# Performance work log

Hardware: AMD Instinct MI355X
Metric: run time of the kernel (lower is better)

## Reference

```python
import jax, jax.numpy as jnp
import numpy as np

L, C = 32768, 512
EPS = 1e-5

def _layernorm(x, w, b):
    mu = jnp.mean(x, axis=-1, keepdims=True)
    var = jnp.mean(jnp.square(x - mu), axis=-1, keepdims=True)
    return (x - mu) * jax.lax.rsqrt(var + EPS) * w + b

def _scan(u, decay):
    # inclusive first-order linear scan: b_t = decay * b_{t-1} + u_t
    a = jnp.broadcast_to(decay, u.shape)
    def combine(l, r):
        return (l[0] * r[0], r[1] + r[0] * l[1])
    _, b = jax.lax.associative_scan(combine, (a, u), axis=0)
    return b

def setup_inputs() -> dict:
    key = jax.random.key(0)
    ks = jax.random.split(key, 8)
    s = 0.02
    return {
        "x": jax.random.normal(ks[0], (L, C), dtype=jnp.float32),
        "ln1_w": jnp.ones((C,), jnp.float32),
        "ln1_b": jnp.zeros((C,), jnp.float32),
        "W_in": jax.random.normal(ks[1], (C, C), jnp.float32) * s,
        "b_in": jnp.zeros((C,), jnp.float32),
        "W_gate": jax.random.normal(ks[2], (C, C), jnp.float32) * s,
        "b_gate": jnp.zeros((C,), jnp.float32),
        "W_out": jax.random.normal(ks[3], (C, C), jnp.float32) * s,
        "b_out": jnp.zeros((C,), jnp.float32),
        "decay_logit": jnp.zeros((C,), jnp.float32),  # torch init: zeros -> sigmoid = 0.5
        "ln2_w": jnp.ones((C,), jnp.float32),
        "ln2_b": jnp.zeros((C,), jnp.float32),
        "W_ff1": jax.random.normal(ks[4], (C, 2 * C), jnp.float32) * s,
        "b_ff1": jnp.zeros((2 * C,), jnp.float32),
        "W_ff2": jax.random.normal(ks[5], (2 * C, C), jnp.float32) * s,
        "b_ff2": jnp.zeros((C,), jnp.float32),
    }

def reference(x, ln1_w, ln1_b, W_in, b_in, W_gate, b_gate, W_out, b_out,
              decay_logit, ln2_w, ln2_b, W_ff1, b_ff1, W_ff2, b_ff2):
    hidden = _layernorm(x, ln1_w, ln1_b)
    u = hidden @ W_in + b_in
    gate = jax.nn.sigmoid(hidden @ W_gate + b_gate)
    decay = jax.nn.sigmoid(decay_logit)
    fwd = _scan(u, decay) * gate
    bwd = jnp.flip(_scan(jnp.flip(u, axis=0), decay), axis=0) * gate
    state_out = 0.5 * (fwd + bwd)
    x = x + state_out @ W_out + b_out
    h = _layernorm(x, ln2_w, ln2_b)
    x = x + jax.nn.silu(h @ W_ff1 + b_ff1) @ W_ff2 + b_ff2
    return x
```

## Files before the change

kernel.cpp:

```cpp
#include <hip/hip_runtime.h>
#include <stdint.h>


#define L_SEQ 32768
#define CDIM 512
#define LN_EPS 1e-5f
#define CHUNK 64
#define NCHUNK (L_SEQ / CHUNK)
#define NGRP 16
#define GCHUNK (NCHUNK / NGRP)

typedef __attribute__((ext_vector_type(8))) short short8;
typedef __attribute__((ext_vector_type(4))) float floatx4;

__device__ inline unsigned short f2bf(float f) {
  union { float f; unsigned int u; } v; v.f = f;
  unsigned int r = v.u + 0x7fffu + ((v.u >> 16) & 1u);
  return (unsigned short)(r >> 16);
}
__device__ inline float bf2f(unsigned short h) {
  union { float f; unsigned int u; } v; v.u = ((unsigned int)h) << 16;
  return v.f;
}
__device__ inline float sigmoidf_(float x) { return 1.0f / (1.0f + __expf(-x)); }

__device__ inline float powi5(float s, int e) {
  float p = 1.f;
#pragma unroll
  for (int b = 0; b < 5; b++) { if (e & (1 << b)) p *= s; s *= s; }
  return p;
}

__device__ __forceinline__ void gll16(const void* g, void* l) {
  __builtin_amdgcn_global_load_lds(
      (__attribute__((address_space(1))) void*)g,
      (__attribute__((address_space(3))) void*)l, 16, 0, 0);
}

__global__ __launch_bounds__(256) void ln_kernel(const float* __restrict__ x,
    const float* __restrict__ w, const float* __restrict__ b,
    unsigned short* __restrict__ out) {
  int row = blockIdx.x * 4 + (threadIdx.x >> 6);
  int lane = threadIdx.x & 63;
  const float4* xr = (const float4*)(x + (size_t)row * CDIM);
  float4 v0 = xr[lane * 2];
  float4 v1 = xr[lane * 2 + 1];
  float s = v0.x + v0.y + v0.z + v0.w + v1.x + v1.y + v1.z + v1.w;
  float s2 = v0.x * v0.x + v0.y * v0.y + v0.z * v0.z + v0.w * v0.w +
             v1.x * v1.x + v1.y * v1.y + v1.z * v1.z + v1.w * v1.w;
  for (int m = 32; m > 0; m >>= 1) {
    s += __shfl_xor(s, m, 64);
    s2 += __shfl_xor(s2, m, 64);
  }
  float mean = s * (1.0f / CDIM);
  float var = s2 * (1.0f / CDIM) - mean * mean;
  float rs = rsqrtf(var + LN_EPS);
  const float4* wr = (const float4*)w;
  const float4* br = (const float4*)b;
  float4 w0 = wr[lane * 2], w1 = wr[lane * 2 + 1];
  float4 b0 = br[lane * 2], b1 = br[lane * 2 + 1];
  unsigned int p0 = (unsigned int)f2bf((v0.x - mean) * rs * w0.x + b0.x) |
                    ((unsigned int)f2bf((v0.y - mean) * rs * w0.y + b0.y) << 16);
  unsigned int p1 = (unsigned int)f2bf((v0.z - mean) * rs * w0.z + b0.z) |
                    ((unsigned int)f2bf((v0.w - mean) * rs * w0.w + b0.w) << 16);
  unsigned int p2 = (unsigned int)f2bf((v1.x - mean) * rs * w1.x + b1.x) |
                    ((unsigned int)f2bf((v1.y - mean) * rs * w1.y + b1.y) << 16);
  unsigned int p3 = (unsigned int)f2bf((v1.z - mean) * rs * w1.z + b1.z) |
                    ((unsigned int)f2bf((v1.w - mean) * rs * w1.w + b1.w) << 16);
  uint4 pk; pk.x = p0; pk.y = p1; pk.z = p2; pk.w = p3;
  *((uint4*)(out + (size_t)row * CDIM + lane * 8)) = pk;
}

__global__ __launch_bounds__(256) void prep_all(
    const float* __restrict__ W_in, const float* __restrict__ W_gate,
    const float* __restrict__ W_out, const float* __restrict__ W_ff1,
    const float* __restrict__ W_ff2, const float* __restrict__ logit,
    unsigned short* __restrict__ Wt_ig, unsigned short* __restrict__ Wt_out,
    unsigned short* __restrict__ Wt_ff1, unsigned short* __restrict__ Wt_ff2,
    float* __restrict__ decay, float* __restrict__ decayT) {
  int b = blockIdx.x;
  if (b >= 1792) {
    for (int c = threadIdx.x; c < CDIM; c += 256) {
      float d = sigmoidf_(logit[c]);
      decay[c] = d;
      float p = d;
      for (int i = 0; i < 6; i++) p *= p;
      decayT[c] = p;
    }
    return;
  }
  const float* W; unsigned short* Wt; int Kd, Nd, t;
  if (b < 256)       { W = W_in;   Wt = Wt_ig;             Kd = 512;  Nd = 512;  t = b; }
  else if (b < 512)  { W = W_gate; Wt = Wt_ig + 512 * 512; Kd = 512;  Nd = 512;  t = b - 256; }
  else if (b < 768)  { W = W_out;  Wt = Wt_out;            Kd = 512;  Nd = 512;  t = b - 512; }
  else if (b < 1280) { W = W_ff1;  Wt = Wt_ff1;            Kd = 512;  Nd = 1024; t = b - 768; }
  else               { W = W_ff2;  Wt = Wt_ff2;            Kd = 1024; Nd = 512;  t = b - 1280; }
  int ntx = Nd >> 5;
  int n0 = (t % ntx) * 32, k0 = (t / ntx) * 32;
  __shared__ float tile[32][33];
  int tx = threadIdx.x & 31, ty = threadIdx.x >> 5;
  for (int r = 0; r < 32; r += 8)
    tile[ty + r][tx] = W[(size_t)(k0 + ty + r) * Nd + n0 + tx];
  __syncthreads();
  for (int r = 0; r < 32; r += 8)
    Wt[(size_t)(n0 + ty + r) * Kd + k0 + tx] = f2bf(tile[tx][ty + r]);
}

template <int EPI>
__global__ __launch_bounds__(256, 4) void gemm_bt(
    const unsigned short* __restrict__ A, const unsigned short* __restrict__ Bt,
    const float* __restrict__ biasA, const float* __restrict__ biasB,
    const float* __restrict__ res, float* __restrict__ outF,
    unsigned short* __restrict__ outU, unsigned short* __restrict__ outG,
    const float* __restrict__ decayP, float* __restrict__ faP,
    float* __restrict__ baP, int M, int N, int K) {
  __shared__ char smemRaw[34048];
  unsigned short* As = (unsigned short*)smemRaw;
  unsigned short* Bs = (unsigned short*)(smemRaw + 16384);

  int nbx = gridDim.x, nby = gridDim.y;
  int bid = blockIdx.x + blockIdx.y * nbx;
  int per = (nbx * nby) >> 3;
  int w = (bid & 7) * per + (bid >> 3);
  int ni = w % nby;
  int mi = w / nby;
  int bm = mi << 7, bn = ni << 7;

  int tid = threadIdx.x, wave = tid >> 6, lane = tid & 63;
  int wm = (wave >> 1) * 64, wn = (wave & 1) * 64;

  int srow = wave * 16 + (lane >> 2);
  int chunkSel = (lane & 3) ^ ((lane >> 3) & 3);
  int scol = chunkSel * 8;
  const unsigned short* aP0 = A + (size_t)(bm + srow) * K + scol;
  const unsigned short* aP1 = A + (size_t)(bm + 64 + srow) * K + scol;
  const unsigned short* bP0 = Bt + (size_t)(bn + srow) * K + scol;
  const unsigned short* bP1 = Bt + (size_t)(bn + 64 + srow) * K + scol;
  int wbase = wave * 512;

#define STAGE(bufOff, ktile) do {                                 \
    int _o = (ktile) * 32;                                        \
    gll16(aP0 + _o, As + (bufOff) + wbase);                       \
    gll16(aP1 + _o, As + (bufOff) + 2048 + wbase);                \
    gll16(bP0 + _o, Bs + (bufOff) + wbase);                       \
    gll16(bP1 + _o, Bs + (bufOff) + 2048 + wbase);                \
  } while (0)

  floatx4 acc[4][4];
#pragma unroll
  for (int i = 0; i < 4; i++)
#pragma unroll
    for (int j = 0; j < 4; j++) acc[i][j] = (floatx4){0.f, 0.f, 0.f, 0.f};

  int quad = lane >> 4, r16 = lane & 15;
  int cSwz = ((quad ^ (r16 >> 1)) & 3) * 8;

  int NK = K >> 5;

  STAGE(0, 0);
  asm volatile("s_waitcnt vmcnt(0)" ::: "memory");
  __syncthreads();

  for (int k = 0; k < NK; ++k) {
    int cur = (k & 1) * 4096, nxt = cur ^ 4096;
    if (k + 1 < NK) STAGE(nxt, k + 1);
    short8 af[4], bfm[4];
#pragma unroll
    for (int i = 0; i < 4; i++)
      af[i] = *(const short8*)(&As[cur + (wm + i * 16 + r16) * 32 + cSwz]);
#pragma unroll
    for (int j = 0; j < 4; j++)
      bfm[j] = *(const short8*)(&Bs[cur + (wn + j * 16 + r16) * 32 + cSwz]);
#pragma unroll
    for (int i = 0; i < 4; i++)
#pragma unroll
      for (int j = 0; j < 4; j++)
        acc[i][j] = __builtin_amdgcn_mfma_f32_16x16x32_bf16(af[i], bfm[j], acc[i][j], 0, 0, 0);
    asm volatile("s_waitcnt vmcnt(0)" ::: "memory");
    __syncthreads();
  }
#undef STAGE

  if (EPI == 1) {
#pragma unroll
    for (int j = 0; j < 4; j++) {
      int n = bn + wn + j * 16 + r16;
#pragma unroll
      for (int i = 0; i < 4; i++) {
        int mb = bm + wm + i * 16 + quad * 4;
#pragma unroll
        for (int r = 0; r < 4; r++) {
          size_t idx = (size_t)(mb + r) * N + n;
          outF[idx] = res[idx] + acc[i][j][r] + biasA[n];
        }
      }
    }
  } else {
    unsigned short* sm = (unsigned short*)smemRaw;
#pragma unroll
    for (int j = 0; j < 4; j++) {
      int n = bn + wn + j * 16 + r16;
      int ln = wn + j * 16 + r16;
#pragma unroll
      for (int i = 0; i < 4; i++) {
        int lmb = wm + i * 16 + quad * 4;
#pragma unroll
        for (int r = 0; r < 4; r++) {
          float v = acc[i][j][r];
          float t;
          if (EPI == 0) {
            t = (n < 512) ? (v + biasA[n]) : sigmoidf_(v + biasB[n - 512]);
          } else {
            float z = v + biasA[n];
            t = z * sigmoidf_(z);
          }
          sm[(lmb + r) * 132 + ln] = f2bf(t);
        }
      }
    }
    __syncthreads();
    int row = tid >> 1, half = tid & 1;
    const unsigned short* src = sm + row * 132 + half * 64;
    unsigned short* gptr;
    if (EPI == 0) {
      gptr = ((bn < 512) ? outU : (outG - 512)) + (size_t)(bm + row) * 512 + bn + half * 64;
    } else {
      gptr = outG + (size_t)(bm + row) * N + bn + half * 64;
    }
#pragma unroll
    for (int s = 0; s < 8; s++)
      *(short8*)(gptr + s * 8) = *(const short8*)(src + s * 8);

    if (EPI == 0 && bn < 512 && faP != nullptr) {
      int cl = tid & 127;
      int ch = tid >> 7;
      int cg = bn + cl;
      float d = decayP[cg];
      const unsigned short* col = sm + (ch * 64) * 132 + cl;
      float f = 0.f, bs = 0.f, p = 1.f;
#pragma unroll 8
      for (int t = 0; t < CHUNK; t++) {
        float v = bf2f(col[t * 132]);
        f = d * f + v;
        bs += p * v;
        p *= d;
      }
      size_t kidx = (size_t)((bm >> 6) + ch) * CDIM + cg;
      faP[kidx] = f;
      baP[kidx] = bs;
    }
  }
}

__global__ __launch_bounds__(512) void scan_p2a(const float* __restrict__ fa,
    const float* __restrict__ ba, const float* __restrict__ decayT,
    float* __restrict__ fc, float* __restrict__ bc,
    float* __restrict__ gaF, float* __restrict__ gaB) {
  int c = threadIdx.x, g = blockIdx.x;
  float dT = decayT[c];
  int k0 = g * GCHUNK;
  float runf = 0.f;
#pragma unroll 4
  for (int j = 0; j < GCHUNK; j++) {
    size_t idx = (size_t)(k0 + j) * CDIM + c;
    fc[idx] = runf;
    runf = dT * runf + fa[idx];
  }
  gaF[(size_t)g * CDIM + c] = runf;
  float runb = 0.f;
#pragma unroll 4
  for (int j = GCHUNK - 1; j >= 0; j--) {
    size_t idx = (size_t)(k0 + j) * CDIM + c;
    bc[idx] = runb;
    runb = dT * runb + ba[idx];
  }
  gaB[(size_t)g * CDIM + c] = runb;
}

__global__ __launch_bounds__(512) void scan_p2b(const float* __restrict__ gaF,
    const float* __restrict__ gaB, const float* __restrict__ decayT,
    float* __restrict__ GF, float* __restrict__ GB) {
  int c = threadIdx.x;
  float dT = decayT[c];
  float d32 = dT;
#pragma unroll
  for (int i = 0; i < 5; i++) d32 *= d32;
  float gf = 0.f;
#pragma unroll
  for (int g = 0; g < NGRP; g++) {
    GF[(size_t)g * CDIM + c] = gf;
    gf = d32 * gf + gaF[(size_t)g * CDIM + c];
  }
  float gb = 0.f;
#pragma unroll
  for (int g = NGRP - 1; g >= 0; g--) {
    GB[(size_t)g * CDIM + c] = gb;
    gb = d32 * gb + gaB[(size_t)g * CDIM + c];
  }
}

__global__ __launch_bounds__(512) void scan_phase3(const unsigned short* __restrict__ u,
    const unsigned short* __restrict__ gate, const float* __restrict__ decay,
    const float* __restrict__ decayT, const float* __restrict__ fc,
    const float* __restrict__ bc, const float* __restrict__ GF,
    const float* __restrict__ GB, unsigned short* __restrict__ state) {
  int c = threadIdx.x, k = blockIdx.x;
  int g = k >> 5, j = k & 31;
  float d = decay[c];
  float dT = decayT[c];
  size_t base = (size_t)k * CHUNK * CDIM + c;
  size_t kc = (size_t)k * CDIM + c;
  size_t gc = (size_t)g * CDIM + c;
  float run  = fc[kc] + powi5(dT, j) * GF[gc];
  float runb0 = bc[kc] + powi5(dT, 31 - j) * GB[gc];
  float fwd[CHUNK];
  unsigned int us[CHUNK / 2];
#pragma unroll
  for (int t = 0; t < CHUNK; t++) {
    unsigned short uv = u[base + (size_t)t * CDIM];
    if (t & 1) us[t >> 1] |= ((unsigned int)uv) << 16;
    else       us[t >> 1] = uv;
    run = d * run + bf2f(uv);
    fwd[t] = run;
  }
  float runb = runb0;
#pragma unroll
  for (int t = CHUNK - 1; t >= 0; t--) {
    unsigned short uv = (unsigned short)((us[t >> 1] >> ((t & 1) * 16)) & 0xffffu);
    runb = d * runb + bf2f(uv);
    float gv = bf2f(gate[base + (size_t)t * CDIM]);
    state[base + (size_t)t * CDIM] = f2bf(0.5f * (fwd[t] + runb) * gv);
  }
}

extern "C" void kernel_launch(void* const* d_in, const int* in_sizes, int n_in,
                              void* d_out, int out_size, void* d_ws, size_t ws_size,
                              hipStream_t stream) {
  const float* x = (const float*)d_in[0];
  const float* ln1_w = (const float*)d_in[1];
  const float* ln1_b = (const float*)d_in[2];
  const float* W_in = (const float*)d_in[3];
  const float* b_in = (const float*)d_in[4];
  const float* W_gate = (const float*)d_in[5];
  const float* b_gate = (const float*)d_in[6];
  const float* W_out = (const float*)d_in[7];
  const float* b_out = (const float*)d_in[8];
  const float* decay_logit = (const float*)d_in[9];
  const float* ln2_w = (const float*)d_in[10];
  const float* ln2_b = (const float*)d_in[11];
  const float* W_ff1 = (const float*)d_in[12];
  const float* b_ff1 = (const float*)d_in[13];
  const float* W_ff2 = (const float*)d_in[14];
  const float* b_ff2 = (const float*)d_in[15];

  char* ws = (char*)d_ws;
  size_t off = 0;
  auto alloc = [&](size_t bytes) -> void* {
    void* p = ws + off;
    off += (bytes + 255) & ~(size_t)255;
    return p;
  };
  unsigned short* Wt_ig  = (unsigned short*)alloc((size_t)1024 * 512 * 2);
  unsigned short* Wt_out = (unsigned short*)alloc((size_t)512 * 512 * 2);
  unsigned short* Wt_ff1 = (unsigned short*)alloc((size_t)1024 * 512 * 2);
  unsigned short* Wt_ff2 = (unsigned short*)alloc((size_t)512 * 1024 * 2);
  float* fa = (float*)alloc((size_t)NCHUNK * CDIM * 4);
  float* ba = (float*)alloc((size_t)NCHUNK * CDIM * 4);
  float* fc = (float*)alloc((size_t)NCHUNK * CDIM * 4);
  float* bc = (float*)alloc((size_t)NCHUNK * CDIM * 4);
  float* gaF = (float*)alloc((size_t)NGRP * CDIM * 4);
  float* gaB = (float*)alloc((size_t)NGRP * CDIM * 4);
  float* GFb = (float*)alloc((size_t)NGRP * CDIM * 4);
  float* GBb = (float*)alloc((size_t)NGRP * CDIM * 4);
  float* decay  = (float*)alloc(CDIM * 4);
  float* decayT = (float*)alloc(CDIM * 4);
  const size_t LC2 = (size_t)L_SEQ * CDIM * 2;
  unsigned short* R1 = (unsigned short*)alloc(LC2);
  unsigned short* R2 = (unsigned short*)alloc(LC2);
  unsigned short* R3 = (unsigned short*)alloc(LC2);
  unsigned short* hidden = R1;
  unsigned short* state  = R1;
  unsigned short* hbuf   = R1;
  unsigned short* u_buf  = R2;
  unsigned short* gate   = R3;
  unsigned short* ffb    = R2;
  float* x2 = (float*)d_out;

  prep_all<<<1793, 256, 0, stream>>>(W_in, W_gate, W_out, W_ff1, W_ff2,
      decay_logit, Wt_ig, Wt_out, Wt_ff1, Wt_ff2, decay, decayT);

  ln_kernel<<<L_SEQ / 4, 256, 0, stream>>>(x, ln1_w, ln1_b, hidden);

  gemm_bt<0><<<dim3(L_SEQ / 128, 1024 / 128), 256, 0, stream>>>(
      hidden, Wt_ig, b_in, b_gate, nullptr, nullptr, u_buf, gate,
      decay, fa, ba, L_SEQ, 1024, 512);

  scan_p2a<<<NGRP, 512, 0, stream>>>(fa, ba, decayT, fc, bc, gaF, gaB);
  scan_p2b<<<1, 512, 0, stream>>>(gaF, gaB, decayT, GFb, GBb);
  scan_phase3<<<NCHUNK, 512, 0, stream>>>(u_buf, gate, decay, decayT, fc, bc,
      GFb, GBb, state);

  gemm_bt<1><<<dim3(L_SEQ / 128, 512 / 128), 256, 0, stream>>>(
      state, Wt_out, b_out, nullptr, x, x2, nullptr, nullptr,
      nullptr, nullptr, nullptr, L_SEQ, 512, 512);

  ln_kernel<<<L_SEQ / 4, 256, 0, stream>>>(x2, ln2_w, ln2_b, hbuf);

  gemm_bt<2><<<dim3(L_SEQ / 128, 1024 / 128), 256, 0, stream>>>(
      hbuf, Wt_ff1, b_ff1, nullptr, nullptr, nullptr, nullptr, ffb,
      nullptr, nullptr, nullptr, L_SEQ, 1024, 512);

  gemm_bt<1><<<dim3(L_SEQ / 128, 512 / 128), 256, 0, stream>>>(
      ffb, Wt_ff2, b_ff2, nullptr, x2, x2, nullptr, nullptr,
      nullptr, nullptr, nullptr, L_SEQ, 512, 1024);
}
```

Before: 424.8 us.

## Store mid-block residual in bf16 and merge LN1 into weight-prep launch

The intermediate residual x2 is now written as bf16 through a staged-LDS epilogue instead of fp32, and LN2 and the final GEMM read it as bf16. This halves the traffic of the residual write and of its two reads. LayerNorm-1 is also folded into the weight-prep kernel as extra blocks, which removes one launch, and the final epilogue hoists the bias load. The cost is reduced precision in the residual stream, which adds rounding error to the output.

```diff
diff --git a/kernel.cpp b/kernel.cpp
--- a/kernel.cpp
+++ b/kernel.cpp
@@ -37,48 +37,49 @@
       (__attribute__((address_space(3))) void*)l, 16, 0, 0);
 }
 
-__global__ __launch_bounds__(256) void ln_kernel(const float* __restrict__ x,
-    const float* __restrict__ w, const float* __restrict__ b,
-    unsigned short* __restrict__ out) {
-  int row = blockIdx.x * 4 + (threadIdx.x >> 6);
-  int lane = threadIdx.x & 63;
-  const float4* xr = (const float4*)(x + (size_t)row * CDIM);
-  float4 v0 = xr[lane * 2];
-  float4 v1 = xr[lane * 2 + 1];
-  float s = v0.x + v0.y + v0.z + v0.w + v1.x + v1.y + v1.z + v1.w;
-  float s2 = v0.x * v0.x + v0.y * v0.y + v0.z * v0.z + v0.w * v0.w +
-             v1.x * v1.x + v1.y * v1.y + v1.z * v1.z + v1.w * v1.w;
-  for (int m = 32; m > 0; m >>= 1) {
-    s += __shfl_xor(s, m, 64);
-    s2 += __shfl_xor(s2, m, 64);
-  }
-  float mean = s * (1.0f / CDIM);
-  float var = s2 * (1.0f / CDIM) - mean * mean;
-  float rs = rsqrtf(var + LN_EPS);
-  const float4* wr = (const float4*)w;
-  const float4* br = (const float4*)b;
-  float4 w0 = wr[lane * 2], w1 = wr[lane * 2 + 1];
-  float4 b0 = br[lane * 2], b1 = br[lane * 2 + 1];
-  unsigned int p0 = (unsigned int)f2bf((v0.x - mean) * rs * w0.x + b0.x) |
-                    ((unsigned int)f2bf((v0.y - mean) * rs * w0.y + b0.y) << 16);
-  unsigned int p1 = (unsigned int)f2bf((v0.z - mean) * rs * w0.z + b0.z) |
-                    ((unsigned int)f2bf((v0.w - mean) * rs * w0.w + b0.w) << 16);
-  unsigned int p2 = (unsigned int)f2bf((v1.x - mean) * rs * w1.x + b1.x) |
-                    ((unsigned int)f2bf((v1.y - mean) * rs * w1.y + b1.y) << 16);
-  unsigned int p3 = (unsigned int)f2bf((v1.z - mean) * rs * w1.z + b1.z) |
-                    ((unsigned int)f2bf((v1.w - mean) * rs * w1.w + b1.w) << 16);
-  uint4 pk; pk.x = p0; pk.y = p1; pk.z = p2; pk.w = p3;
-  *((uint4*)(out + (size_t)row * CDIM + lane * 8)) = pk;
-}
-
-__global__ __launch_bounds__(256) void prep_all(
+__global__ __launch_bounds__(256) void prep_ln1(
+    const float* __restrict__ x, const float* __restrict__ ln1_w,
+    const float* __restrict__ ln1_b, unsigned short* __restrict__ out,
     const float* __restrict__ W_in, const float* __restrict__ W_gate,
     const float* __restrict__ W_out, const float* __restrict__ W_ff1,
     const float* __restrict__ W_ff2, const float* __restrict__ logit,
     unsigned short* __restrict__ Wt_ig, unsigned short* __restrict__ Wt_out,
     unsigned short* __restrict__ Wt_ff1, unsigned short* __restrict__ Wt_ff2,
     float* __restrict__ decay, float* __restrict__ decayT) {
-  int b = blockIdx.x;
+  int bx = blockIdx.x;
+  if (bx < L_SEQ / 4) {
+    int row = bx * 4 + (threadIdx.x >> 6);
+    int lane = threadIdx.x & 63;
+    const float4* xr = (const float4*)(x + (size_t)row * CDIM);
+    float4 v0 = xr[lane * 2];
+    float4 v1 = xr[lane * 2 + 1];
+    float s = v0.x + v0.y + v0.z + v0.w + v1.x + v1.y + v1.z + v1.w;
+    float s2 = v0.x * v0.x + v0.y * v0.y + v0.z * v0.z + v0.w * v0.w +
+               v1.x * v1.x + v1.y * v1.y + v1.z * v1.z + v1.w * v1.w;
+    for (int m = 32; m > 0; m >>= 1) {
+      s += __shfl_xor(s, m, 64);
+      s2 += __shfl_xor(s2, m, 64);
+    }
+    float mean = s * (1.0f / CDIM);
+    float var = s2 * (1.0f / CDIM) - mean * mean;
+    float rs = rsqrtf(var + LN_EPS);
+    const float4* wr = (const float4*)ln1_w;
+    const float4* br = (const float4*)ln1_b;
+    float4 w0 = wr[lane * 2], w1 = wr[lane * 2 + 1];
+    float4 b0 = br[lane * 2], b1 = br[lane * 2 + 1];
+    unsigned int p0 = (unsigned int)f2bf((v0.x - mean) * rs * w0.x + b0.x) |
+                      ((unsigned int)f2bf((v0.y - mean) * rs * w0.y + b0.y) << 16);
+    unsigned int p1 = (unsigned int)f2bf((v0.z - mean) * rs * w0.z + b0.z) |
+                      ((unsigned int)f2bf((v0.w - mean) * rs * w0.w + b0.w) << 16);
+    unsigned int p2 = (unsigned int)f2bf((v1.x - mean) * rs * w1.x + b1.x) |
+                      ((unsigned int)f2bf((v1.y - mean) * rs * w1.y + b1.y) << 16);
+    unsigned int p3 = (unsigned int)f2bf((v1.z - mean) * rs * w1.z + b1.z) |
+                      ((unsigned int)f2bf((v1.w - mean) * rs * w1.w + b1.w) << 16);
+    uint4 pk; pk.x = p0; pk.y = p1; pk.z = p2; pk.w = p3;
+    *((uint4*)(out + (size_t)row * CDIM + lane * 8)) = pk;
+    return;
+  }
+  int b = bx - L_SEQ / 4;
   if (b >= 1792) {
     for (int c = threadIdx.x; c < CDIM; c += 256) {
       float d = sigmoidf_(logit[c]);
@@ -106,11 +107,53 @@
     Wt[(size_t)(n0 + ty + r) * Kd + k0 + tx] = f2bf(tile[tx][ty + r]);
 }
 
+__global__ __launch_bounds__(256) void ln_bf16(const unsigned short* __restrict__ xb,
+    const float* __restrict__ w, const float* __restrict__ b,
+    unsigned short* __restrict__ out) {
+  int row = blockIdx.x * 4 + (threadIdx.x >> 6);
+  int lane = threadIdx.x & 63;
+  uint4 uv = *(const uint4*)(xb + (size_t)row * CDIM + lane * 8);
+  float v[8];
+  v[0] = bf2f((unsigned short)(uv.x & 0xffffu));
+  v[1] = bf2f((unsigned short)(uv.x >> 16));
+  v[2] = bf2f((unsigned short)(uv.y & 0xffffu));
+  v[3] = bf2f((unsigned short)(uv.y >> 16));
+  v[4] = bf2f((unsigned short)(uv.z & 0xffffu));
+  v[5] = bf2f((unsigned short)(uv.z >> 16));
+  v[6] = bf2f((unsigned short)(uv.w & 0xffffu));
+  v[7] = bf2f((unsigned short)(uv.w >> 16));
+  float s = 0.f, s2 = 0.f;
+#pragma unroll
+  for (int i = 0; i < 8; i++) { s += v[i]; s2 += v[i] * v[i]; }
+  for (int m = 32; m > 0; m >>= 1) {
+    s += __shfl_xor(s, m, 64);
+    s2 += __shfl_xor(s2, m, 64);
+  }
+  float mean = s * (1.0f / CDIM);
+  float var = s2 * (1.0f / CDIM) - mean * mean;
+  float rs = rsqrtf(var + LN_EPS);
+  const float4* wr = (const float4*)w;
+  const float4* br = (const float4*)b;
+  float4 w0 = wr[lane * 2], w1 = wr[lane * 2 + 1];
+  float4 b0 = br[lane * 2], b1 = br[lane * 2 + 1];
+  unsigned int p0 = (unsigned int)f2bf((v[0] - mean) * rs * w0.x + b0.x) |
+                    ((unsigned int)f2bf((v[1] - mean) * rs * w0.y + b0.y) << 16);
+  unsigned int p1 = (unsigned int)f2bf((v[2] - mean) * rs * w0.z + b0.z) |
+                    ((unsigned int)f2bf((v[3] - mean) * rs * w0.w + b0.w) << 16);
+  unsigned int p2 = (unsigned int)f2bf((v[4] - mean) * rs * w1.x + b1.x) |
+                    ((unsigned int)f2bf((v[5] - mean) * rs * w1.y + b1.y) << 16);
+  unsigned int p3 = (unsigned int)f2bf((v[6] - mean) * rs * w1.z + b1.z) |
+                    ((unsigned int)f2bf((v[7] - mean) * rs * w1.w + b1.w) << 16);
+  uint4 pk; pk.x = p0; pk.y = p1; pk.z = p2; pk.w = p3;
+  *((uint4*)(out + (size_t)row * CDIM + lane * 8)) = pk;
+}
+
 template <int EPI>
 __global__ __launch_bounds__(256, 4) void gemm_bt(
     const unsigned short* __restrict__ A, const unsigned short* __restrict__ Bt,
     const float* __restrict__ biasA, const float* __restrict__ biasB,
-    const float* __restrict__ res, float* __restrict__ outF,
+    const float* __restrict__ res, const unsigned short* __restrict__ resB,
+    float* __restrict__ outF,
     unsigned short* __restrict__ outU, unsigned short* __restrict__ outG,
     const float* __restrict__ decayP, float* __restrict__ faP,
     float* __restrict__ baP, int M, int N, int K) {
@@ -181,17 +224,18 @@
   }
 #undef STAGE
 
-  if (EPI == 1) {
+  if (EPI == 4) {
 #pragma unroll
     for (int j = 0; j < 4; j++) {
       int n = bn + wn + j * 16 + r16;
+      float bA = biasA[n];
 #pragma unroll
       for (int i = 0; i < 4; i++) {
         int mb = bm + wm + i * 16 + quad * 4;
 #pragma unroll
         for (int r = 0; r < 4; r++) {
           size_t idx = (size_t)(mb + r) * N + n;
-          outF[idx] = res[idx] + acc[i][j][r] + biasA[n];
+          outF[idx] = bf2f(resB[idx]) + acc[i][j][r] + bA;
         }
       }
     }
@@ -210,9 +254,12 @@
           float t;
           if (EPI == 0) {
             t = (n < 512) ? (v + biasA[n]) : sigmoidf_(v + biasB[n - 512]);
-          } else {
+          } else if (EPI == 2) {
             float z = v + biasA[n];
             t = z * sigmoidf_(z);
+          } else {
+            size_t gidx = (size_t)(bm + lmb + r) * N + n;
+            t = res[gidx] + v + biasA[n];
           }
           sm[(lmb + r) * 132 + ln] = f2bf(t);
         }
@@ -378,21 +425,20 @@
   unsigned short* R1 = (unsigned short*)alloc(LC2);
   unsigned short* R2 = (unsigned short*)alloc(LC2);
   unsigned short* R3 = (unsigned short*)alloc(LC2);
+  unsigned short* x2b = (unsigned short*)alloc(LC2);
   unsigned short* hidden = R1;
   unsigned short* state  = R1;
   unsigned short* hbuf   = R1;
   unsigned short* u_buf  = R2;
   unsigned short* gate   = R3;
   unsigned short* ffb    = R2;
-  float* x2 = (float*)d_out;
-
-  prep_all<<<1793, 256, 0, stream>>>(W_in, W_gate, W_out, W_ff1, W_ff2,
-      decay_logit, Wt_ig, Wt_out, Wt_ff1, Wt_ff2, decay, decayT);
-
-  ln_kernel<<<L_SEQ / 4, 256, 0, stream>>>(x, ln1_w, ln1_b, hidden);
+
+  prep_ln1<<<L_SEQ / 4 + 1793, 256, 0, stream>>>(x, ln1_w, ln1_b, hidden,
+      W_in, W_gate, W_out, W_ff1, W_ff2, decay_logit,
+      Wt_ig, Wt_out, Wt_ff1, Wt_ff2, decay, decayT);
 
   gemm_bt<0><<<dim3(L_SEQ / 128, 1024 / 128), 256, 0, stream>>>(
-      hidden, Wt_ig, b_in, b_gate, nullptr, nullptr, u_buf, gate,
+      hidden, Wt_ig, b_in, b_gate, nullptr, nullptr, nullptr, u_buf, gate,
       decay, fa, ba, L_SEQ, 1024, 512);
 
   scan_p2a<<<NGRP, 512, 0, stream>>>(fa, ba, decayT, fc, bc, gaF, gaB);
@@ -400,17 +446,17 @@
   scan_phase3<<<NCHUNK, 512, 0, stream>>>(u_buf, gate, decay, decayT, fc, bc,
       GFb, GBb, state);
 
-  gemm_bt<1><<<dim3(L_SEQ / 128, 512 / 128), 256, 0, stream>>>(
-      state, Wt_out, b_out, nullptr, x, x2, nullptr, nullptr,
+  gemm_bt<3><<<dim3(L_SEQ / 128, 512 / 128), 256, 0, stream>>>(
+      state, Wt_out, b_out, nullptr, x, nullptr, nullptr, nullptr, x2b,
       nullptr, nullptr, nullptr, L_SEQ, 512, 512);
 
-  ln_kernel<<<L_SEQ / 4, 256, 0, stream>>>(x2, ln2_w, ln2_b, hbuf);
+  ln_bf16<<<L_SEQ / 4, 256, 0, stream>>>(x2b, ln2_w, ln2_b, hbuf);
 
   gemm_bt<2><<<dim3(L_SEQ / 128, 1024 / 128), 256, 0, stream>>>(
-      hbuf, Wt_ff1, b_ff1, nullptr, nullptr, nullptr, nullptr, ffb,
+      hbuf, Wt_ff1, b_ff1, nullptr, nullptr, nullptr, nullptr, nullptr, ffb,
       nullptr, nullptr, nullptr, L_SEQ, 1024, 512);
 
-  gemm_bt<1><<<dim3(L_SEQ / 128, 512 / 128), 256, 0, stream>>>(
-      ffb, Wt_ff2, b_ff2, nullptr, x2, x2, nullptr, nullptr,
+  gemm_bt<4><<<dim3(L_SEQ / 128, 512 / 128), 256, 0, stream>>>(
+      ffb, Wt_ff2, b_ff2, nullptr, nullptr, x2b, (float*)d_out, nullptr, nullptr,
       nullptr, nullptr, nullptr, L_SEQ, 512, 1024);
 }
```

Result: faster. 411.0 us (-3.3%).
